# Performance work log

Hardware: AMD Instinct MI355X
Metric: run time of the kernel (lower is better)

## Reference

```python
import jax, jax.numpy as jnp
import numpy as np

EPSILON = 0.01
NITER = 100
N = 16
THRESH = 0.1  # 10**-1
LOSS_WEIGHT = 10.0
D = 65536


def setup_inputs() -> dict:
    key = jax.random.key(0)
    k1, k2 = jax.random.split(key)
    preds_S = jax.random.normal(k1, (N, D), dtype=jnp.float32)
    preds_T = jax.random.normal(k2, (N, D), dtype=jnp.float32)
    return {"preds_S": preds_S, "preds_T": preds_T}


def _sinkhorn_loss(x, y):
    # cost matrix C_ij = sum_k |x_ik - y_jk|^2  -> [N, N]
    C = jnp.sum(jnp.abs(x[:, None, :] - y[None, :, :]) ** 2, axis=2)
    mu = jnp.full((N,), 1.0 / N, dtype=x.dtype)
    nu = jnp.full((N,), 1.0 / N, dtype=x.dtype)
    log_mu = jnp.log(mu)
    log_nu = jnp.log(nu)

    def M(u, v):
        # modified cost (-C + u_i + v_j) / epsilon
        return (-C + u[:, None] + v[None, :]) / EPSILON

    def lse(A):
        # faithful to the torch code: log(sum(exp(A), axis=1) + 1e-6)
        return jnp.log(jnp.sum(jnp.exp(A), axis=1) + 1e-6)

    def body(carry, _):
        u, v, done = carry
        u1 = u
        u_new = EPSILON * (log_mu - lse(M(u, v))) + u
        v_new = EPSILON * (log_nu - lse(M(u_new, v).T)) + v
        err = jnp.sum(jnp.abs(u_new - u1))
        # early-exit emulation: once converged, freeze state (iteration where
        # err < thresh still applies its update, matching the torch break)
        u = jnp.where(done, u, u_new)
        v = jnp.where(done, v, v_new)
        done = done | (err < THRESH)
        return (u, v, done), None

    u0 = jnp.zeros((N,), dtype=x.dtype)
    v0 = jnp.zeros((N,), dtype=x.dtype)
    (u, v, _), _ = jax.lax.scan(body, (u0, v0, jnp.array(False)), None, length=NITER)

    pi = jnp.exp(M(u, v))
    return jnp.sum(pi * C)


def reference(preds_S, preds_T):
    # forward uses sinkhorn_loss(preds_S, preds_S, ...); preds_T is unused
    loss = _sinkhorn_loss(preds_S, preds_S)
    return LOSS_WEIGHT * loss
```

## Files before the change

kernel.cpp:

```cpp
#include <hip/hip_runtime.h>

#define NN 16
#define DD 65536
#define DD4 (DD / 4)
#define NPAIR 120
#define NCHUNK 8
#define CHUNK4 (DD4 / NCHUNK)
#define EPS 0.01f
#define NITERS 100
#define THRESH 0.1f

__global__ __launch_bounds__(256) void sumsq_pairs_kernel(
    const float* __restrict__ x, float* __restrict__ partial) {
    int b = blockIdx.x;
    int pair = b >> 3;
    int chunk = b & 7;
    int i = 0, p = pair;
    while (p >= 15 - i) { p -= 15 - i; ++i; }
    int j = i + 1 + p;

    const float4* xi = (const float4*)(x + (size_t)i * DD);
    const float4* xj = (const float4*)(x + (size_t)j * DD);

    int base = chunk * CHUNK4;
    float acc = 0.0f;
    #pragma unroll 4
    for (int k = base + threadIdx.x; k < base + CHUNK4; k += 256) {
        float4 a = xi[k];
        float4 c = xj[k];
        float d0 = a.x - c.x, d1 = a.y - c.y, d2 = a.z - c.z, d3 = a.w - c.w;
        acc += d0 * d0 + d1 * d1 + d2 * d2 + d3 * d3;
    }
    #pragma unroll
    for (int m = 32; m >= 1; m >>= 1) acc += __shfl_xor(acc, m, 64);

    __shared__ float sred[4];
    int lane = threadIdx.x & 63;
    int wv = threadIdx.x >> 6;
    if (lane == 0) sred[wv] = acc;
    __syncthreads();
    if (threadIdx.x == 0)
        partial[b] = ((sred[0] + sred[1]) + sred[2]) + sred[3];
}

__global__ __launch_bounds__(256) void sinkhorn_kernel(
    const float* __restrict__ partial, float* __restrict__ out) {
    __shared__ float sC[NN * 17];
    __shared__ float su[NN], sv[NN], su_new[NN], sv_new[NN], sdu[NN];
    __shared__ float serr;
    __shared__ float sred[4];

    int tid = threadIdx.x;

    if (tid < NN) {
        su[tid] = 0.0f;
        sv[tid] = 0.0f;
        sC[tid * 17 + tid] = 0.0f;
    }
    if (tid < NPAIR) {
        int i = 0, p = tid;
        while (p >= 15 - i) { p -= 15 - i; ++i; }
        int j = i + 1 + p;
        float s = 0.0f;
        #pragma unroll
        for (int c = 0; c < NCHUNK; ++c) s += partial[tid * NCHUNK + c];
        sC[i * 17 + j] = s;
        sC[j * 17 + i] = s;
    }
    __syncthreads();

    const float log_mu = logf(1.0f / 16.0f);

    int i_r = tid >> 4, j_r = tid & 15;
    int i_c = tid & 15, j_c = tid >> 4;

    for (int it = 0; it < NITERS; ++it) {
        float e = expf((-sC[i_r * 17 + j_r] + su[i_r] + sv[j_r]) / EPS);
        e += __shfl_xor(e, 1, 64);
        e += __shfl_xor(e, 2, 64);
        e += __shfl_xor(e, 4, 64);
        e += __shfl_xor(e, 8, 64);
        if (j_r == 0) {
            float lse = logf(e + 1e-6f);
            float un = EPS * (log_mu - lse) + su[i_r];
            su_new[i_r] = un;
            sdu[i_r] = fabsf(un - su[i_r]);
        }
        __syncthreads();

        float e2 = expf((-sC[i_c * 17 + j_c] + su_new[i_c] + sv[j_c]) / EPS);
        e2 += __shfl_xor(e2, 1, 64);
        e2 += __shfl_xor(e2, 2, 64);
        e2 += __shfl_xor(e2, 4, 64);
        e2 += __shfl_xor(e2, 8, 64);
        if (i_c == 0) {
            float lse = logf(e2 + 1e-6f);
            sv_new[j_c] = EPS * (log_mu - lse) + sv[j_c];
        }
        __syncthreads();

        if (tid == 0) {
            float err = 0.0f;
            #pragma unroll
            for (int k = 0; k < NN; ++k) err += sdu[k];
            serr = err;
        }
        if (tid < NN) {
            su[tid] = su_new[tid];
            sv[tid] = sv_new[tid];
        }
        __syncthreads();
        if (serr < THRESH) break;
    }

    float c = sC[i_r * 17 + j_r];
    float term = expf((-c + su[i_r] + sv[j_r]) / EPS) * c;
    #pragma unroll
    for (int m = 32; m >= 1; m >>= 1) term += __shfl_xor(term, m, 64);
    if ((tid & 63) == 0) sred[tid >> 6] = term;
    __syncthreads();
    if (tid == 0)
        out[0] = 10.0f * (((sred[0] + sred[1]) + sred[2]) + sred[3]);
}

extern "C" void kernel_launch(void* const* d_in, const int* in_sizes, int n_in,
                              void* d_out, int out_size, void* d_ws, size_t ws_size,
                              hipStream_t stream) {
    const float* preds_S = (const float*)d_in[0];
    float* partial = (float*)d_ws;
    float* out = (float*)d_out;

    hipLaunchKernelGGL(sumsq_pairs_kernel, dim3(NPAIR * NCHUNK), dim3(256), 0, stream,
                       preds_S, partial);
    hipLaunchKernelGGL(sinkhorn_kernel, dim3(1), dim3(256), 0, stream,
                       partial, out);
}
```

Baseline: 13.59 us.

## Compute pairwise distances via Gram matrix with single-pass column-tiled loads

```diff
diff --git a/kernel.cpp b/kernel.cpp
--- a/kernel.cpp
+++ b/kernel.cpp
@@ -3,48 +3,90 @@
 #define NN 16
 #define DD 65536
 #define DD4 (DD / 4)
-#define NPAIR 120
-#define NCHUNK 8
-#define CHUNK4 (DD4 / NCHUNK)
+#define BBLK 256
+#define COLS_PER_BLK (DD4 / BBLK)
+#define NITEM 136
+#define ITEMS_PER_WAVE 34
 #define EPS 0.01f
 #define NITERS 100
 #define THRESH 0.1f
 
-__global__ __launch_bounds__(256) void sumsq_pairs_kernel(
+constexpr int item_i(int it) {
+    if (it < NN) return it;
+    int p = it - NN, i = 0;
+    while (p >= 15 - i) { p -= 15 - i; ++i; }
+    return i;
+}
+constexpr int item_j(int it) {
+    if (it < NN) return it;
+    int p = it - NN, i = 0;
+    while (p >= 15 - i) { p -= 15 - i; ++i; }
+    return i + 1 + p;
+}
+
+template <int... Ks> struct IntSeq {};
+template <int N, int... S> struct MakeSeq : MakeSeq<N - 1, N - 1, S...> {};
+template <int... S> struct MakeSeq<0, S...> { using type = IntSeq<S...>; };
+
+template <int IT, int K>
+__device__ __forceinline__ void acc_one(const float4 (&r)[NN], float (&acc)[ITEMS_PER_WAVE]) {
+    constexpr int I = item_i(IT);
+    constexpr int J = item_j(IT);
+    float4 a = r[I], b = r[J];
+    acc[K] = fmaf(a.w, b.w, fmaf(a.z, b.z, fmaf(a.y, b.y, fmaf(a.x, b.x, acc[K]))));
+}
+
+template <int W, int... Ks>
+__device__ __forceinline__ void acc_wave(const float4 (&r)[NN], float (&acc)[ITEMS_PER_WAVE],
+                                         IntSeq<Ks...>) {
+    (acc_one<W * ITEMS_PER_WAVE + Ks, Ks>(r, acc), ...);
+}
+
+__global__ __launch_bounds__(256) void partial_kernel(
     const float* __restrict__ x, float* __restrict__ partial) {
-    int b = blockIdx.x;
-    int pair = b >> 3;
-    int chunk = b & 7;
-    int i = 0, p = pair;
-    while (p >= 15 - i) { p -= 15 - i; ++i; }
-    int j = i + 1 + p;
+    int wave = threadIdx.x >> 6;
+    int lane = threadIdx.x & 63;
+    int col = blockIdx.x * COLS_PER_BLK + lane;
 
-    const float4* xi = (const float4*)(x + (size_t)i * DD);
-    const float4* xj = (const float4*)(x + (size_t)j * DD);
+    const float4* x4 = (const float4*)x;
+    float4 r[NN];
+    #pragma unroll
+    for (int row = 0; row < NN; ++row) r[row] = x4[row * DD4 + col];
 
-    int base = chunk * CHUNK4;
-    float acc = 0.0f;
-    #pragma unroll 4
-    for (int k = base + threadIdx.x; k < base + CHUNK4; k += 256) {
-        float4 a = xi[k];
-        float4 c = xj[k];
-        float d0 = a.x - c.x, d1 = a.y - c.y, d2 = a.z - c.z, d3 = a.w - c.w;
-        acc += d0 * d0 + d1 * d1 + d2 * d2 + d3 * d3;
+    float acc[ITEMS_PER_WAVE];
+    #pragma unroll
+    for (int k = 0; k < ITEMS_PER_WAVE; ++k) acc[k] = 0.0f;
+
+    using Seq = MakeSeq<ITEMS_PER_WAVE>::type;
+    switch (wave) {
+        case 0: acc_wave<0>(r, acc, Seq{}); break;
+        case 1: acc_wave<1>(r, acc, Seq{}); break;
+        case 2: acc_wave<2>(r, acc, Seq{}); break;
+        default: acc_wave<3>(r, acc, Seq{}); break;
     }
+
     #pragma unroll
-    for (int m = 32; m >= 1; m >>= 1) acc += __shfl_xor(acc, m, 64);
+    for (int k = 0; k < ITEMS_PER_WAVE; ++k) {
+        float v = acc[k];
+        v += __shfl_xor(v, 1, 64);
+        v += __shfl_xor(v, 2, 64);
+        v += __shfl_xor(v, 4, 64);
+        v += __shfl_xor(v, 8, 64);
+        v += __shfl_xor(v, 16, 64);
+        v += __shfl_xor(v, 32, 64);
+        acc[k] = v;
+    }
 
-    __shared__ float sred[4];
-    int lane = threadIdx.x & 63;
-    int wv = threadIdx.x >> 6;
-    if (lane == 0) sred[wv] = acc;
-    __syncthreads();
-    if (threadIdx.x == 0)
-        partial[b] = ((sred[0] + sred[1]) + sred[2]) + sred[3];
+    if (lane == 0) {
+        #pragma unroll
+        for (int k = 0; k < ITEMS_PER_WAVE; ++k)
+            partial[(wave * ITEMS_PER_WAVE + k) * BBLK + blockIdx.x] = acc[k];
+    }
 }
 
 __global__ __launch_bounds__(256) void sinkhorn_kernel(
     const float* __restrict__ partial, float* __restrict__ out) {
+    __shared__ float sItem[NITEM];
     __shared__ float sC[NN * 17];
     __shared__ float su[NN], sv[NN], su_new[NN], sv_new[NN], sdu[NN];
     __shared__ float serr;
@@ -52,21 +94,30 @@
 
     int tid = threadIdx.x;
 
-    if (tid < NN) {
-        su[tid] = 0.0f;
-        sv[tid] = 0.0f;
-        sC[tid * 17 + tid] = 0.0f;
+    if (tid < NITEM) {
+        const float4* p4 = (const float4*)(partial + tid * BBLK);
+        float s0 = 0.f, s1 = 0.f, s2 = 0.f, s3 = 0.f;
+        #pragma unroll
+        for (int b = 0; b < BBLK / 4; ++b) {
+            float4 v = p4[b];
+            s0 += v.x; s1 += v.y; s2 += v.z; s3 += v.w;
+        }
+        sItem[tid] = (s0 + s1) + (s2 + s3);
     }
-    if (tid < NPAIR) {
-        int i = 0, p = tid;
-        while (p >= 15 - i) { p -= 15 - i; ++i; }
-        int j = i + 1 + p;
-        float s = 0.0f;
-        #pragma unroll
-        for (int c = 0; c < NCHUNK; ++c) s += partial[tid * NCHUNK + c];
-        sC[i * 17 + j] = s;
-        sC[j * 17 + i] = s;
+    __syncthreads();
+
+    {
+        int ci = tid >> 4, cj = tid & 15;
+        float c = 0.0f;
+        if (ci != cj) {
+            int i = ci < cj ? ci : cj;
+            int j = ci < cj ? cj : ci;
+            int p = i * 15 - i * (i - 1) / 2 + (j - i - 1);
+            c = sItem[i] + sItem[j] - 2.0f * sItem[NN + p];
+        }
+        sC[ci * 17 + cj] = c;
     }
+    if (tid < NN) { su[tid] = 0.0f; sv[tid] = 0.0f; }
     __syncthreads();
 
     const float log_mu = logf(1.0f / 16.0f);
@@ -130,7 +181,7 @@
     float* partial = (float*)d_ws;
     float* out = (float*)d_out;
 
-    hipLaunchKernelGGL(sumsq_pairs_kernel, dim3(NPAIR * NCHUNK), dim3(256), 0, stream,
+    hipLaunchKernelGGL(partial_kernel, dim3(BBLK), dim3(256), 0, stream,
                        preds_S, partial);
     hipLaunchKernelGGL(sinkhorn_kernel, dim3(1), dim3(256), 0, stream,
                        partial, out);
```

New measurement: 18.94 us. 39.4% more time.

## Fuse pairwise distance and Sinkhorn kernels using an in-kernel spin-wait handoff

Applied to the files above, without the earlier changes.

```diff
diff --git a/kernel.cpp b/kernel.cpp
--- a/kernel.cpp
+++ b/kernel.cpp
@@ -1,4 +1,5 @@
 #include <hip/hip_runtime.h>
+#include <stdint.h>
 
 #define NN 16
 #define DD 65536
@@ -6,51 +7,72 @@
 #define NPAIR 120
 #define NCHUNK 8
 #define CHUNK4 (DD4 / NCHUNK)
+#define NPROD (NPAIR * NCHUNK)
+#define XKEY 0xDEADBEEFu
 #define EPS 0.01f
 #define NITERS 100
 #define THRESH 0.1f
 
-__global__ __launch_bounds__(256) void sumsq_pairs_kernel(
-    const float* __restrict__ x, float* __restrict__ partial) {
-    int b = blockIdx.x;
-    int pair = b >> 3;
-    int chunk = b & 7;
-    int i = 0, p = pair;
-    while (p >= 15 - i) { p -= 15 - i; ++i; }
-    int j = i + 1 + p;
-
-    const float4* xi = (const float4*)(x + (size_t)i * DD);
-    const float4* xj = (const float4*)(x + (size_t)j * DD);
-
-    int base = chunk * CHUNK4;
-    float acc = 0.0f;
-    #pragma unroll 4
-    for (int k = base + threadIdx.x; k < base + CHUNK4; k += 256) {
-        float4 a = xi[k];
-        float4 c = xj[k];
-        float d0 = a.x - c.x, d1 = a.y - c.y, d2 = a.z - c.z, d3 = a.w - c.w;
-        acc += d0 * d0 + d1 * d1 + d2 * d2 + d3 * d3;
-    }
-    #pragma unroll
-    for (int m = 32; m >= 1; m >>= 1) acc += __shfl_xor(acc, m, 64);
-
+__global__ __launch_bounds__(256) void sinkhorn_fused_kernel(
+    const float* __restrict__ x, uint32_t* __restrict__ ws0,
+    uint32_t* __restrict__ ws1, float* __restrict__ out) {
     __shared__ float sred[4];
-    int lane = threadIdx.x & 63;
-    int wv = threadIdx.x >> 6;
-    if (lane == 0) sred[wv] = acc;
-    __syncthreads();
-    if (threadIdx.x == 0)
-        partial[b] = ((sred[0] + sred[1]) + sred[2]) + sred[3];
-}
-
-__global__ __launch_bounds__(256) void sinkhorn_kernel(
-    const float* __restrict__ partial, float* __restrict__ out) {
+    __shared__ float sp[NPROD];
     __shared__ float sC[NN * 17];
     __shared__ float su[NN], sv[NN], su_new[NN], sv_new[NN], sdu[NN];
     __shared__ float serr;
-    __shared__ float sred[4];
 
     int tid = threadIdx.x;
+
+    if (blockIdx.x < NPROD) {
+        int b = blockIdx.x;
+        int pair = b >> 3;
+        int chunk = b & 7;
+        int i = 0, p = pair;
+        while (p >= 15 - i) { p -= 15 - i; ++i; }
+        int j = i + 1 + p;
+
+        const float4* xi = (const float4*)(x + (size_t)i * DD);
+        const float4* xj = (const float4*)(x + (size_t)j * DD);
+
+        int base = chunk * CHUNK4;
+        float acc = 0.0f;
+        #pragma unroll 4
+        for (int k = base + tid; k < base + CHUNK4; k += 256) {
+            float4 a = xi[k];
+            float4 c = xj[k];
+            float d0 = a.x - c.x, d1 = a.y - c.y, d2 = a.z - c.z, d3 = a.w - c.w;
+            acc += d0 * d0 + d1 * d1 + d2 * d2 + d3 * d3;
+        }
+        #pragma unroll
+        for (int m = 32; m >= 1; m >>= 1) acc += __shfl_xor(acc, m, 64);
+
+        int lane = tid & 63;
+        int wv = tid >> 6;
+        if (lane == 0) sred[wv] = acc;
+        __syncthreads();
+        if (tid == 0) {
+            float s = ((sred[0] + sred[1]) + sred[2]) + sred[3];
+            uint32_t bits = __float_as_uint(s);
+            __hip_atomic_store(ws0 + b, bits, __ATOMIC_RELAXED,
+                               __HIP_MEMORY_SCOPE_AGENT);
+            __hip_atomic_store(ws1 + b, bits ^ XKEY, __ATOMIC_RELAXED,
+                               __HIP_MEMORY_SCOPE_AGENT);
+        }
+        return;
+    }
+
+    for (int b = tid; b < NPROD; b += 256) {
+        uint32_t w0, w1;
+        do {
+            w0 = __hip_atomic_load(ws0 + b, __ATOMIC_RELAXED,
+                                   __HIP_MEMORY_SCOPE_AGENT);
+            w1 = __hip_atomic_load(ws1 + b, __ATOMIC_RELAXED,
+                                   __HIP_MEMORY_SCOPE_AGENT);
+        } while (w1 != (w0 ^ XKEY));
+        sp[b] = __uint_as_float(w0);
+    }
+    __syncthreads();
 
     if (tid < NN) {
         su[tid] = 0.0f;
@@ -63,7 +85,7 @@
         int j = i + 1 + p;
         float s = 0.0f;
         #pragma unroll
-        for (int c = 0; c < NCHUNK; ++c) s += partial[tid * NCHUNK + c];
+        for (int c = 0; c < NCHUNK; ++c) s += sp[tid * NCHUNK + c];
         sC[i * 17 + j] = s;
         sC[j * 17 + i] = s;
     }
@@ -127,11 +149,10 @@
                               void* d_out, int out_size, void* d_ws, size_t ws_size,
                               hipStream_t stream) {
     const float* preds_S = (const float*)d_in[0];
-    float* partial = (float*)d_ws;
+    uint32_t* ws0 = (uint32_t*)d_ws;
+    uint32_t* ws1 = ws0 + NPROD;
     float* out = (float*)d_out;
 
-    hipLaunchKernelGGL(sumsq_pairs_kernel, dim3(NPAIR * NCHUNK), dim3(256), 0, stream,
-                       preds_S, partial);
-    hipLaunchKernelGGL(sinkhorn_kernel, dim3(1), dim3(256), 0, stream,
-                       partial, out);
+    hipLaunchKernelGGL(sinkhorn_fused_kernel, dim3(NPROD + 1), dim3(256), 0, stream,
+                       preds_S, ws0, ws1, out);
 }
```

New measurement: 12.88 us. 1.05x faster.
